# Kernel optimization log

Measured on AMD Instinct MI355X. Metric: run time of the kernel, lower is better.

Reference implementation:

```python
import jax, jax.numpy as jnp
import numpy as np
import math

B, L, D, H, FF = 4, 1024, 1024, 16, 4096
DH = D // H
EPS = 1e-12


def layer_norm(x, gamma, beta):
    mean = x.mean(-1, keepdims=True)
    var = ((x - mean) ** 2).mean(-1, keepdims=True)  # biased var, matches unbiased=False
    return gamma * (x - mean) / jnp.sqrt(var + EPS) + beta


def setup_inputs() -> dict:
    key = jax.random.key(0)
    ks = jax.random.split(key, 16)
    s = 0.02
    return {
        "x": jax.random.normal(ks[0], (B, L, D), jnp.float32),
        "attn_bias": jax.random.uniform(ks[1], (B, L, L), jnp.float32),
        "src_mask": jax.random.randint(ks[2], (B, L), 0, 2, jnp.int32),
        "wq": jax.random.normal(ks[3], (D, D), jnp.float32) * s,
        "bq": jnp.zeros((D,), jnp.float32),
        "wk": jax.random.normal(ks[4], (D, D), jnp.float32) * s,
        "bk": jnp.zeros((D,), jnp.float32),
        "wv": jax.random.normal(ks[5], (D, D), jnp.float32) * s,
        "bv": jnp.zeros((D,), jnp.float32),
        "wo": jax.random.normal(ks[6], (D, D), jnp.float32) * s,
        "bo": jnp.zeros((D,), jnp.float32),
        "gamma1": jnp.ones((D,), jnp.float32),
        "beta1": jnp.zeros((D,), jnp.float32),
        "w1": jax.random.normal(ks[7], (D, FF), jnp.float32) * s,
        "b1": jnp.zeros((FF,), jnp.float32),
        "w2": jax.random.normal(ks[8], (FF, D), jnp.float32) * s,
        "b2": jnp.zeros((D,), jnp.float32),
        "gamma2": jnp.ones((D,), jnp.float32),
        "beta2": jnp.zeros((D,), jnp.float32),
    }


def reference(x, attn_bias, src_mask, wq, bq, wk, bk, wv, bv, wo, bo,
              gamma1, beta1, w1, b1, w2, b2, gamma2, beta2):
    # ---- multi-head attention with multiplicative bias + additive mask ----
    def split_heads(t):  # [B,L,D] -> [B,H,L,DH]
        return t.reshape(B, L, H, DH).transpose(0, 2, 1, 3)

    q = split_heads(x @ wq + bq)
    k = split_heads(x @ wk + bk)
    v = split_heads(x @ wv + bv)

    score = jnp.einsum('bhqd,bhkd->bhqk', q, k) / math.sqrt(DH)
    score = score * attn_bias[:, None, :, :]               # multiplicative bias
    score = jnp.where(src_mask[:, None, None, :] == 0, -10000.0, score)
    p = jax.nn.softmax(score, axis=-1)
    ctx = jnp.einsum('bhqk,bhkd->bhqd', p, v)
    ctx = ctx.transpose(0, 2, 1, 3).reshape(B, L, D)
    attn_out = ctx @ wo + bo

    h = layer_norm(x + attn_out, gamma1, beta1)

    # ---- position-wise FFN ----
    ffn = jax.nn.relu(h @ w1 + b1) @ w2 + b2
    out = layer_norm(h + ffn, gamma2, beta2)
    return out
```

## Files before the change

kernel.cpp:

```cpp
#include <hip/hip_runtime.h>
#include <hip/hip_bf16.h>
#include <math.h>

#define BB 4
#define LL 1024
#define DD 1024
#define HH 16
#define DHH 64
#define FFF 4096
#define MM (BB*LL)
#define LDQ 3072

typedef __attribute__((ext_vector_type(8))) short short8;
typedef __attribute__((ext_vector_type(4))) float f32x4;

__device__ __forceinline__ ushort f2bf(float f) {
    __hip_bfloat16 h = __float2bfloat16(f);
    return *(ushort*)&h;
}
__device__ __forceinline__ float bf2f(ushort u) {
    __hip_bfloat16 h = *(__hip_bfloat16*)&u;
    return __bfloat162float(h);
}

__device__ __forceinline__ float block_reduce_sum(float v, float* red, int tid) {
    red[tid] = v;
    __syncthreads();
    for (int off = 128; off > 0; off >>= 1) {
        if (tid < off) red[tid] += red[tid + off];
        __syncthreads();
    }
    float r = red[0];
    __syncthreads();
    return r;
}

__global__ __launch_bounds__(256)
void cast_bf16(const float* __restrict__ in, ushort* __restrict__ out) {
    const int i = blockIdx.x * 256 + threadIdx.x;
    float4 v = ((const float4*)in)[i];
    ushort4 o;
    o.x = f2bf(v.x); o.y = f2bf(v.y); o.z = f2bf(v.z); o.w = f2bf(v.w);
    ((ushort4*)out)[i] = o;
}

__global__ __launch_bounds__(256)
void transpose_cast(const float* __restrict__ W, ushort* __restrict__ WT,
                    int K, int N) {
    __shared__ float tile[32][33];
    const int n0 = blockIdx.x * 32, k0 = blockIdx.y * 32;
    const int t = threadIdx.x;
    const int r = t >> 3, c4 = (t & 7) * 4;
    float4 v = *(const float4*)&W[(size_t)(k0 + r) * N + n0 + c4];
    tile[r][c4 + 0] = v.x; tile[r][c4 + 1] = v.y;
    tile[r][c4 + 2] = v.z; tile[r][c4 + 3] = v.w;
    __syncthreads();
    ushort4 o;
    o.x = f2bf(tile[c4 + 0][r]);
    o.y = f2bf(tile[c4 + 1][r]);
    o.z = f2bf(tile[c4 + 2][r]);
    o.w = f2bf(tile[c4 + 3][r]);
    *(ushort4*)&WT[(size_t)(n0 + r) * K + k0 + c4] = o;
}

__global__ __launch_bounds__(256)
void concat3(const float* __restrict__ a, const float* __restrict__ b,
             const float* __restrict__ c, float* __restrict__ o) {
    const int i = blockIdx.x * 256 + threadIdx.x;
    o[i] = (i < 1024) ? a[i] : ((i < 2048) ? b[i - 1024] : c[i - 2048]);
}

template<int BN>
__global__ __launch_bounds__(256)
void gemm_bf16(const ushort* __restrict__ A, const ushort* __restrict__ Bt,
               const float* __restrict__ bias, void* __restrict__ C,
               ushort* __restrict__ Vt, int vn0,
               int M, int N, int K, int relu, int obf16, int qlim) {
    constexpr int JF = BN / 32;
    __shared__ ushort Als0[128 * 32];
    __shared__ ushort Als1[128 * 32];
    __shared__ ushort Bls0[BN * 32];
    __shared__ ushort Bls1[BN * 32];

    const int L = blockIdx.x + gridDim.x * blockIdx.y;
    const int xcd = L & 7;
    const int idx = L >> 3;
    const int mpx = gridDim.y >> 3;
    const int bm = (xcd * mpx + (idx % mpx)) * 128;
    const int bn = (idx / mpx) * BN;

    const int t = threadIdx.x;
    const int lane = t & 63;
    const int w = t >> 6;
    const int wm = (w >> 1) * 64;
    const int wn = (w & 1) * (BN / 2);
    const int fm = lane & 15;
    const int kg = lane >> 4;

    f32x4 acc[4][JF] = {};

    for (int k0 = 0; k0 < K; k0 += 64) {
        #pragma unroll
        for (int j = 0; j < 2; ++j) {
            const int chunk = j * 256 + t;
            const int row = chunk >> 2, kc = chunk & 3;
            const ushort* ga0 = A + (size_t)(bm + row) * K + k0 + kc * 8;
            __builtin_amdgcn_global_load_lds(
                (const __attribute__((address_space(1))) void*)ga0,
                (__attribute__((address_space(3))) void*)(Als0 + chunk * 8), 16, 0, 0);
            const ushort* ga1 = ga0 + 32;
            __builtin_amdgcn_global_load_lds(
                (const __attribute__((address_space(1))) void*)ga1,
                (__attribute__((address_space(3))) void*)(Als1 + chunk * 8), 16, 0, 0);
        }
        #pragma unroll
        for (int j = 0; j < BN / 64; ++j) {
            const int chunk = j * 256 + t;
            const int row = chunk >> 2, kc = chunk & 3;
            const ushort* gb0 = Bt + (size_t)(bn + row) * K + k0 + kc * 8;
            __builtin_amdgcn_global_load_lds(
                (const __attribute__((address_space(1))) void*)gb0,
                (__attribute__((address_space(3))) void*)(Bls0 + chunk * 8), 16, 0, 0);
            const ushort* gb1 = gb0 + 32;
            __builtin_amdgcn_global_load_lds(
                (const __attribute__((address_space(1))) void*)gb1,
                (__attribute__((address_space(3))) void*)(Bls1 + chunk * 8), 16, 0, 0);
        }
        __syncthreads();

        short8 af[4][2], bfr[JF][2];
        #pragma unroll
        for (int i = 0; i < 4; ++i) {
            af[i][0] = *(const short8*)&Als0[(wm + i * 16 + fm) * 32 + kg * 8];
            af[i][1] = *(const short8*)&Als1[(wm + i * 16 + fm) * 32 + kg * 8];
        }
        #pragma unroll
        for (int j = 0; j < JF; ++j) {
            bfr[j][0] = *(const short8*)&Bls0[(wn + j * 16 + fm) * 32 + kg * 8];
            bfr[j][1] = *(const short8*)&Bls1[(wn + j * 16 + fm) * 32 + kg * 8];
        }
        #pragma unroll
        for (int i = 0; i < 4; ++i)
            #pragma unroll
            for (int j = 0; j < JF; ++j) {
                acc[i][j] = __builtin_amdgcn_mfma_f32_16x16x32_bf16(
                    af[i][0], bfr[j][0], acc[i][j], 0, 0, 0);
                acc[i][j] = __builtin_amdgcn_mfma_f32_16x16x32_bf16(
                    af[i][1], bfr[j][1], acc[i][j], 0, 0, 0);
            }
        __syncthreads();
    }

    const int orow0 = (lane >> 4) * 4;
    const int ocol = lane & 15;
    #pragma unroll
    for (int j = 0; j < JF; ++j) {
        const int n = bn + wn + j * 16 + ocol;
        const float bv = bias[n];
        const bool isV = (bn + wn + j * 16) >= vn0;
        #pragma unroll
        for (int i = 0; i < 4; ++i) {
            const int m0 = bm + wm + i * 16 + orow0;
            if (isV) {
                ushort4 o;
                float v0 = acc[i][j][0] + bv, v1 = acc[i][j][1] + bv;
                float v2 = acc[i][j][2] + bv, v3 = acc[i][j][3] + bv;
                o.x = f2bf(v0); o.y = f2bf(v1); o.z = f2bf(v2); o.w = f2bf(v3);
                *(ushort4*)&Vt[((size_t)((m0 >> 10) << 10) + (n - vn0)) * 1024 + (m0 & 1023)] = o;
            } else {
                #pragma unroll
                for (int r = 0; r < 4; ++r) {
                    const int m = m0 + r;
                    float v = acc[i][j][r] + bv;
                    if (relu) v = fmaxf(v, 0.0f);
                    if (n < qlim) v *= 0.125f;
                    if (obf16)
                        ((ushort*)C)[(size_t)m * N + n] = f2bf(v);
                    else
                        ((float*)C)[(size_t)m * N + n] = v;
                }
            }
        }
    }
}

__global__ __launch_bounds__(256, 2)
void attn_mfma(const ushort* __restrict__ QKVb, const ushort* __restrict__ Vt,
               const ushort* __restrict__ biasb, const int* __restrict__ mask,
               ushort* __restrict__ ctx) {
    const int q0 = blockIdx.x * 128;
    const int h = blockIdx.y;
    const int b = blockIdx.z;
    const int t = threadIdx.x;
    const int lane = t & 63;
    const int w = t >> 6;
    const int g = lane >> 4;
    const int c = lane & 15;

    __shared__ ushort Qs[128 * 72];
    __shared__ ushort Ks[64 * 72];
    __shared__ ushort Vs[64 * 72];
    __shared__ ushort Bs[128 * 72];
    __shared__ ushort Ps[4][32 * 72];
    __shared__ int maskS[LL];

    #pragma unroll
    for (int i = 0; i < 4; ++i) {
        const int chunk = i * 256 + t;
        const int row = chunk >> 3, c8 = (chunk & 7) * 8;
        *(short8*)&Qs[row * 72 + c8] =
            *(const short8*)(QKVb + ((size_t)(b * LL + q0 + row)) * LDQ + h * DHH + c8);
    }
    ((int4*)maskS)[t] = ((const int4*)(mask + b * LL))[t];

    short8 pk[2], pv[2], pb[4];
    #pragma unroll
    for (int i = 0; i < 2; ++i) {
        const int chunk = i * 256 + t;
        const int row = chunk >> 3, c8 = (chunk & 7) * 8;
        pk[i] = *(const short8*)(QKVb + ((size_t)(b * LL + row)) * LDQ + 1024 + h * DHH + c8);
        pv[i] = *(const short8*)(Vt + ((size_t)((b * HH + h) * DHH + row)) * LL + c8);
    }
    #pragma unroll
    for (int i = 0; i < 4; ++i) {
        const int chunk = i * 256 + t;
        const int row = chunk >> 3, c8 = (chunk & 7) * 8;
        pb[i] = *(const short8*)(biasb + ((size_t)(b * LL + q0 + row)) * LL + c8);
    }
    __syncthreads();

    short8 aq[2][2];
    #pragma unroll
    for (int p = 0; p < 2; ++p) {
        aq[p][0] = *(const short8*)&Qs[(w * 32 + p * 16 + c) * 72 + g * 8];
        aq[p][1] = *(const short8*)&Qs[(w * 32 + p * 16 + c) * 72 + g * 8 + 32];
    }

    float m_pr[2][4], l_run[2][4];
    f32x4 acc_o[2][4] = {};
    #pragma unroll
    for (int p = 0; p < 2; ++p)
        #pragma unroll
        for (int r = 0; r < 4; ++r) { m_pr[p][r] = -3.4e38f; l_run[p][r] = 0.0f; }

    for (int kt = 0; kt < 16; ++kt) {
        #pragma unroll
        for (int i = 0; i < 2; ++i) {
            const int chunk = i * 256 + t;
            const int row = chunk >> 3, c8 = (chunk & 7) * 8;
            *(short8*)&Ks[row * 72 + c8] = pk[i];
            *(short8*)&Vs[row * 72 + c8] = pv[i];
        }
        #pragma unroll
        for (int i = 0; i < 4; ++i) {
            const int chunk = i * 256 + t;
            const int row = chunk >> 3, c8 = (chunk & 7) * 8;
            *(short8*)&Bs[row * 72 + c8] = pb[i];
        }
        __syncthreads();

        if (kt < 15) {
            const int k0n = (kt + 1) * 64;
            #pragma unroll
            for (int i = 0; i < 2; ++i) {
                const int chunk = i * 256 + t;
                const int row = chunk >> 3, c8 = (chunk & 7) * 8;
                pk[i] = *(const short8*)(QKVb + ((size_t)(b * LL + k0n + row)) * LDQ + 1024 + h * DHH + c8);
                pv[i] = *(const short8*)(Vt + ((size_t)((b * HH + h) * DHH + row)) * LL + k0n + c8);
            }
            #pragma unroll
            for (int i = 0; i < 4; ++i) {
                const int chunk = i * 256 + t;
                const int row = chunk >> 3, c8 = (chunk & 7) * 8;
                pb[i] = *(const short8*)(biasb + ((size_t)(b * LL + q0 + row)) * LL + k0n + c8);
            }
        }
        const int k0 = kt * 64;

        f32x4 accs[2][4] = {};
        #pragma unroll
        for (int j = 0; j < 4; ++j) {
            short8 bk0 = *(const short8*)&Ks[(j * 16 + c) * 72 + g * 8];
            short8 bk1 = *(const short8*)&Ks[(j * 16 + c) * 72 + g * 8 + 32];
            #pragma unroll
            for (int p = 0; p < 2; ++p) {
                accs[p][j] = __builtin_amdgcn_mfma_f32_16x16x32_bf16(aq[p][0], bk0, accs[p][j], 0, 0, 0);
                accs[p][j] = __builtin_amdgcn_mfma_f32_16x16x32_bf16(aq[p][1], bk1, accs[p][j], 0, 0, 0);
            }
        }

        int mk[4];
        #pragma unroll
        for (int j = 0; j < 4; ++j) mk[j] = maskS[k0 + j * 16 + c];

        #pragma unroll
        for (int p = 0; p < 2; ++p) {
            float sc[4][4];
            #pragma unroll
            for (int j = 0; j < 4; ++j)
                #pragma unroll
                for (int r = 0; r < 4; ++r) {
                    const float bw = bf2f(Bs[(w * 32 + p * 16 + 4 * g + r) * 72 + j * 16 + c]);
                    float v = accs[p][j][r] * bw;
                    sc[j][r] = (mk[j] == 0) ? -10000.0f : v;
                }

            float mt[4];
            #pragma unroll
            for (int r = 0; r < 4; ++r)
                mt[r] = fmaxf(fmaxf(sc[0][r], sc[1][r]), fmaxf(sc[2][r], sc[3][r]));
            #pragma unroll
            for (int d = 1; d < 16; d <<= 1)
                #pragma unroll
                for (int r = 0; r < 4; ++r)
                    mt[r] = fmaxf(mt[r], __shfl_xor(mt[r], d));

            float al[4], lt[4];
            #pragma unroll
            for (int r = 0; r < 4; ++r) {
                float mn = fmaxf(m_pr[p][r], mt[r]);
                al[r] = __expf(m_pr[p][r] - mn);
                m_pr[p][r] = mn;
                lt[r] = 0.0f;
            }

            #pragma unroll
            for (int j = 0; j < 4; ++j)
                #pragma unroll
                for (int r = 0; r < 4; ++r) {
                    float pe = __expf(sc[j][r] - m_pr[p][r]);
                    lt[r] += pe;
                    Ps[w][(p * 16 + 4 * g + r) * 72 + j * 16 + c] = f2bf(pe);
                }
            #pragma unroll
            for (int d = 1; d < 16; d <<= 1)
                #pragma unroll
                for (int r = 0; r < 4; ++r)
                    lt[r] += __shfl_xor(lt[r], d);
            #pragma unroll
            for (int r = 0; r < 4; ++r)
                l_run[p][r] = l_run[p][r] * al[r] + lt[r];

            #pragma unroll
            for (int j = 0; j < 4; ++j)
                #pragma unroll
                for (int r = 0; r < 4; ++r)
                    acc_o[p][j][r] *= al[r];
        }

        #pragma unroll
        for (int ks = 0; ks < 2; ++ks) {
            short8 ap[2];
            #pragma unroll
            for (int p = 0; p < 2; ++p)
                ap[p] = *(const short8*)&Ps[w][(p * 16 + c) * 72 + ks * 32 + g * 8];
            #pragma unroll
            for (int j = 0; j < 4; ++j) {
                short8 bv8 = *(const short8*)&Vs[(j * 16 + c) * 72 + ks * 32 + g * 8];
                #pragma unroll
                for (int p = 0; p < 2; ++p)
                    acc_o[p][j] = __builtin_amdgcn_mfma_f32_16x16x32_bf16(ap[p], bv8, acc_o[p][j], 0, 0, 0);
            }
        }
        __syncthreads();
    }

    #pragma unroll
    for (int p = 0; p < 2; ++p)
        #pragma unroll
        for (int r = 0; r < 4; ++r) {
            const float inv = 1.0f / l_run[p][r];
            #pragma unroll
            for (int j = 0; j < 4; ++j)
                ctx[((size_t)(b * LL + q0 + w * 32 + p * 16 + 4 * g + r)) * DD + h * DHH + j * 16 + c] =
                    f2bf(acc_o[p][j][r] * inv);
        }
}

__global__ __launch_bounds__(256)
void add_ln_kernel(const float* __restrict__ a, const float* __restrict__ bres,
                   const float* __restrict__ gamma, const float* __restrict__ beta,
                   float* __restrict__ out, ushort* __restrict__ outb) {
    const int row = blockIdx.x;
    const int tid = threadIdx.x;
    __shared__ float red[256];

    const size_t base = (size_t)row * DD;
    float v[4];
    float sum = 0.0f;
    #pragma unroll
    for (int i = 0; i < 4; ++i) {
        const int col = tid + i * 256;
        v[i] = a[base + col] + bres[base + col];
        sum += v[i];
    }
    const float mean = block_reduce_sum(sum, red, tid) * (1.0f / 1024.0f);
    float vs = 0.0f;
    #pragma unroll
    for (int i = 0; i < 4; ++i) {
        const float dlt = v[i] - mean;
        vs += dlt * dlt;
    }
    const float var = block_reduce_sum(vs, red, tid) * (1.0f / 1024.0f);
    const float rstd = rsqrtf(var + 1e-12f);
    #pragma unroll
    for (int i = 0; i < 4; ++i) {
        const int col = tid + i * 256;
        const float o = gamma[col] * (v[i] - mean) * rstd + beta[col];
        out[base + col] = o;
        if (outb) outb[base + col] = f2bf(o);
    }
}

extern "C" void kernel_launch(void* const* d_in, const int* in_sizes, int n_in,
                              void* d_out, int out_size, void* d_ws, size_t ws_size,
                              hipStream_t stream) {
    const float* x         = (const float*)d_in[0];
    const float* attn_bias = (const float*)d_in[1];
    const int*   src_mask  = (const int*)  d_in[2];
    const float* wq = (const float*)d_in[3];
    const float* bq = (const float*)d_in[4];
    const float* wk = (const float*)d_in[5];
    const float* bk = (const float*)d_in[6];
    const float* wv = (const float*)d_in[7];
    const float* bv = (const float*)d_in[8];
    const float* wo = (const float*)d_in[9];
    const float* bo = (const float*)d_in[10];
    const float* gamma1 = (const float*)d_in[11];
    const float* beta1  = (const float*)d_in[12];
    const float* w1 = (const float*)d_in[13];
    const float* b1 = (const float*)d_in[14];
    const float* w2 = (const float*)d_in[15];
    const float* b2 = (const float*)d_in[16];
    const float* gamma2 = (const float*)d_in[17];
    const float* beta2  = (const float*)d_in[18];
    float* out = (float*)d_out;

    const size_t MB = 1024 * 1024;
    char* W = (char*)d_ws;
    ushort* xb    = (ushort*)(W + 0);
    ushort* ctxb  = (ushort*)(W + 0);
    ushort* QKVb  = (ushort*)(W + 8 * MB);
    ushort* F1b   = (ushort*)(W + 8 * MB);
    ushort* Vt    = (ushort*)(W + 40 * MB);
    ushort* W1T   = (ushort*)(W + 40 * MB);
    ushort* WQKVT = (ushort*)(W + 48 * MB);
    ushort* WOT   = (ushort*)(W + 48 * MB);
    ushort* Hbb   = (ushort*)(W + 54 * MB);
    ushort* W2T   = (ushort*)(W + 54 * MB);
    float*  bqkv  = (float*) (W + 62 * MB);
    ushort* biasb = (ushort*)(W + 64 * MB);
    float*  Ao    = (float*) (W + 64 * MB);
    float*  F2    = (float*) (W + 64 * MB);
    float*  Hb    = (float*) (W + 80 * MB);

    dim3 blk(256);

    cast_bf16<<<dim3(4096), blk, 0, stream>>>(x, xb);
    cast_bf16<<<dim3(4096), blk, 0, stream>>>(attn_bias, biasb);
    transpose_cast<<<dim3(32, 32), blk, 0, stream>>>(wq, WQKVT, DD, DD);
    transpose_cast<<<dim3(32, 32), blk, 0, stream>>>(wk, WQKVT + 1024 * 1024, DD, DD);
    transpose_cast<<<dim3(32, 32), blk, 0, stream>>>(wv, WQKVT + 2048 * 1024, DD, DD);
    concat3<<<dim3(12), blk, 0, stream>>>(bq, bk, bv, bqkv);
    gemm_bf16<128><<<dim3(24, 32), blk, 0, stream>>>(xb, WQKVT, bqkv, QKVb,
                                                     Vt, 2048, MM, LDQ, DD, 0, 1, 1024);
    attn_mfma<<<dim3(8, HH, BB), blk, 0, stream>>>(QKVb, Vt, biasb, src_mask, ctxb);
    transpose_cast<<<dim3(32, 32), blk, 0, stream>>>(wo, WOT, DD, DD);
    gemm_bf16<64><<<dim3(16, 32), blk, 0, stream>>>(ctxb, WOT, bo, Ao,
                                                    Vt, 1 << 30, MM, DD, DD, 0, 0, 0);
    add_ln_kernel<<<dim3(MM), blk, 0, stream>>>(Ao, x, gamma1, beta1, Hb, Hbb);
    transpose_cast<<<dim3(128, 32), blk, 0, stream>>>(w1, W1T, DD, FFF);
    gemm_bf16<128><<<dim3(32, 32), blk, 0, stream>>>(Hbb, W1T, b1, F1b,
                                                     Vt, 1 << 30, MM, FFF, DD, 1, 1, 0);
    transpose_cast<<<dim3(32, 128), blk, 0, stream>>>(w2, W2T, FFF, DD);
    gemm_bf16<64><<<dim3(16, 32), blk, 0, stream>>>(F1b, W2T, b2, F2,
                                                    Vt, 1 << 30, MM, DD, FFF, 0, 0, 0);
    add_ln_kernel<<<dim3(MM), blk, 0, stream>>>(F2, Hb, gamma2, beta2, out, nullptr);
}
```

Measured before the change: 419.8 us.

## Swizzle attention bias to fragment order and halve attention query tile

```diff
diff --git a/kernel.cpp b/kernel.cpp
--- a/kernel.cpp
+++ b/kernel.cpp
@@ -22,6 +22,13 @@
     __hip_bfloat16 h = *(__hip_bfloat16*)&u;
     return __bfloat162float(h);
 }
+__device__ __forceinline__ float fexp2(float x) {
+#if __has_builtin(__builtin_amdgcn_exp2f)
+    return __builtin_amdgcn_exp2f(x);
+#else
+    return exp2f(x);
+#endif
+}
 
 __device__ __forceinline__ float block_reduce_sum(float v, float* red, int tid) {
     red[tid] = v;
@@ -42,6 +49,23 @@
     ushort4 o;
     o.x = f2bf(v.x); o.y = f2bf(v.y); o.z = f2bf(v.z); o.w = f2bf(v.w);
     ((ushort4*)out)[i] = o;
+}
+
+__global__ __launch_bounds__(256)
+void swizzle_bias(const float* __restrict__ bias, ushort* __restrict__ B) {
+    __shared__ float rowbuf[1024];
+    const int row = blockIdx.x;
+    const int t = threadIdx.x;
+    *(float4*)&rowbuf[t * 4] = *(const float4*)&bias[(size_t)row * 1024 + t * 4];
+    __syncthreads();
+    const int kt = t >> 4, c = t & 15;
+    const float s = 1.4426950408889634f;
+    ushort4 o;
+    o.x = f2bf(rowbuf[kt * 64 + 0 * 16 + c] * s);
+    o.y = f2bf(rowbuf[kt * 64 + 1 * 16 + c] * s);
+    o.z = f2bf(rowbuf[kt * 64 + 2 * 16 + c] * s);
+    o.w = f2bf(rowbuf[kt * 64 + 3 * 16 + c] * s);
+    *(ushort4*)&B[(size_t)row * 1024 + t * 4] = o;
 }
 
 __global__ __launch_bounds__(256)
@@ -184,11 +208,11 @@
     }
 }
 
-__global__ __launch_bounds__(256, 2)
+__global__ __launch_bounds__(256, 3)
 void attn_mfma(const ushort* __restrict__ QKVb, const ushort* __restrict__ Vt,
-               const ushort* __restrict__ biasb, const int* __restrict__ mask,
+               const ushort* __restrict__ biasw, const int* __restrict__ mask,
                ushort* __restrict__ ctx) {
-    const int q0 = blockIdx.x * 128;
+    const int q0 = blockIdx.x * 64;
     const int h = blockIdx.y;
     const int b = blockIdx.z;
     const int t = threadIdx.x;
@@ -197,23 +221,21 @@
     const int g = lane >> 4;
     const int c = lane & 15;
 
-    __shared__ ushort Qs[128 * 72];
+    __shared__ ushort QP[64 * 72];
     __shared__ ushort Ks[64 * 72];
     __shared__ ushort Vs[64 * 72];
-    __shared__ ushort Bs[128 * 72];
-    __shared__ ushort Ps[4][32 * 72];
     __shared__ int maskS[LL];
 
     #pragma unroll
-    for (int i = 0; i < 4; ++i) {
+    for (int i = 0; i < 2; ++i) {
         const int chunk = i * 256 + t;
         const int row = chunk >> 3, c8 = (chunk & 7) * 8;
-        *(short8*)&Qs[row * 72 + c8] =
+        *(short8*)&QP[row * 72 + c8] =
             *(const short8*)(QKVb + ((size_t)(b * LL + q0 + row)) * LDQ + h * DHH + c8);
     }
     ((int4*)maskS)[t] = ((const int4*)(mask + b * LL))[t];
 
-    short8 pk[2], pv[2], pb[4];
+    short8 pk[2], pv[2];
     #pragma unroll
     for (int i = 0; i < 2; ++i) {
         const int chunk = i * 256 + t;
@@ -221,27 +243,15 @@
         pk[i] = *(const short8*)(QKVb + ((size_t)(b * LL + row)) * LDQ + 1024 + h * DHH + c8);
         pv[i] = *(const short8*)(Vt + ((size_t)((b * HH + h) * DHH + row)) * LL + c8);
     }
-    #pragma unroll
-    for (int i = 0; i < 4; ++i) {
-        const int chunk = i * 256 + t;
-        const int row = chunk >> 3, c8 = (chunk & 7) * 8;
-        pb[i] = *(const short8*)(biasb + ((size_t)(b * LL + q0 + row)) * LL + c8);
-    }
     __syncthreads();
 
-    short8 aq[2][2];
-    #pragma unroll
-    for (int p = 0; p < 2; ++p) {
-        aq[p][0] = *(const short8*)&Qs[(w * 32 + p * 16 + c) * 72 + g * 8];
-        aq[p][1] = *(const short8*)&Qs[(w * 32 + p * 16 + c) * 72 + g * 8 + 32];
-    }
-
-    float m_pr[2][4], l_run[2][4];
-    f32x4 acc_o[2][4] = {};
-    #pragma unroll
-    for (int p = 0; p < 2; ++p)
-        #pragma unroll
-        for (int r = 0; r < 4; ++r) { m_pr[p][r] = -3.4e38f; l_run[p][r] = 0.0f; }
+    short8 aq0 = *(const short8*)&QP[(w * 16 + c) * 72 + g * 8];
+    short8 aq1 = *(const short8*)&QP[(w * 16 + c) * 72 + g * 8 + 32];
+    ushort* Pw = QP + w * (16 * 72);
+
+    float m_pr[4] = {-3.4e38f, -3.4e38f, -3.4e38f, -3.4e38f};
+    float l_run[4] = {0.f, 0.f, 0.f, 0.f};
+    f32x4 acc_o[4] = {};
 
     for (int kt = 0; kt < 16; ++kt) {
         #pragma unroll
@@ -251,12 +261,6 @@
             *(short8*)&Ks[row * 72 + c8] = pk[i];
             *(short8*)&Vs[row * 72 + c8] = pv[i];
         }
-        #pragma unroll
-        for (int i = 0; i < 4; ++i) {
-            const int chunk = i * 256 + t;
-            const int row = chunk >> 3, c8 = (chunk & 7) * 8;
-            *(short8*)&Bs[row * 72 + c8] = pb[i];
-        }
         __syncthreads();
 
         if (kt < 15) {
@@ -268,113 +272,102 @@
                 pk[i] = *(const short8*)(QKVb + ((size_t)(b * LL + k0n + row)) * LDQ + 1024 + h * DHH + c8);
                 pv[i] = *(const short8*)(Vt + ((size_t)((b * HH + h) * DHH + row)) * LL + k0n + c8);
             }
-            #pragma unroll
-            for (int i = 0; i < 4; ++i) {
-                const int chunk = i * 256 + t;
-                const int row = chunk >> 3, c8 = (chunk & 7) * 8;
-                pb[i] = *(const short8*)(biasb + ((size_t)(b * LL + q0 + row)) * LL + k0n + c8);
-            }
-        }
-        const int k0 = kt * 64;
-
-        f32x4 accs[2][4] = {};
+        }
+
+        ushort4 pb[4];
+        #pragma unroll
+        for (int r = 0; r < 4; ++r) {
+            const int q = q0 + w * 16 + 4 * g + r;
+            pb[r] = *(const ushort4*)&biasw[((size_t)(b * LL + q) * 16 + kt) * 64 + c * 4];
+        }
+        int mk[4];
+        #pragma unroll
+        for (int j = 0; j < 4; ++j) mk[j] = maskS[kt * 64 + j * 16 + c];
+
+        f32x4 accs[4] = {};
         #pragma unroll
         for (int j = 0; j < 4; ++j) {
             short8 bk0 = *(const short8*)&Ks[(j * 16 + c) * 72 + g * 8];
             short8 bk1 = *(const short8*)&Ks[(j * 16 + c) * 72 + g * 8 + 32];
-            #pragma unroll
-            for (int p = 0; p < 2; ++p) {
-                accs[p][j] = __builtin_amdgcn_mfma_f32_16x16x32_bf16(aq[p][0], bk0, accs[p][j], 0, 0, 0);
-                accs[p][j] = __builtin_amdgcn_mfma_f32_16x16x32_bf16(aq[p][1], bk1, accs[p][j], 0, 0, 0);
-            }
-        }
-
-        int mk[4];
-        #pragma unroll
-        for (int j = 0; j < 4; ++j) mk[j] = maskS[k0 + j * 16 + c];
-
-        #pragma unroll
-        for (int p = 0; p < 2; ++p) {
-            float sc[4][4];
-            #pragma unroll
-            for (int j = 0; j < 4; ++j)
-                #pragma unroll
-                for (int r = 0; r < 4; ++r) {
-                    const float bw = bf2f(Bs[(w * 32 + p * 16 + 4 * g + r) * 72 + j * 16 + c]);
-                    float v = accs[p][j][r] * bw;
-                    sc[j][r] = (mk[j] == 0) ? -10000.0f : v;
-                }
-
-            float mt[4];
+            accs[j] = __builtin_amdgcn_mfma_f32_16x16x32_bf16(aq0, bk0, accs[j], 0, 0, 0);
+            accs[j] = __builtin_amdgcn_mfma_f32_16x16x32_bf16(aq1, bk1, accs[j], 0, 0, 0);
+        }
+
+        float sc[4][4];
+        #pragma unroll
+        for (int j = 0; j < 4; ++j)
+            #pragma unroll
+            for (int r = 0; r < 4; ++r) {
+                const float bw = bf2f(((const ushort*)&pb[r])[j]);
+                const float v = accs[j][r] * bw;
+                sc[j][r] = (mk[j] == 0) ? -14427.0f : v;
+            }
+
+        float mt[4];
+        #pragma unroll
+        for (int r = 0; r < 4; ++r)
+            mt[r] = fmaxf(fmaxf(sc[0][r], sc[1][r]), fmaxf(sc[2][r], sc[3][r]));
+        #pragma unroll
+        for (int d = 1; d < 16; d <<= 1)
             #pragma unroll
             for (int r = 0; r < 4; ++r)
-                mt[r] = fmaxf(fmaxf(sc[0][r], sc[1][r]), fmaxf(sc[2][r], sc[3][r]));
-            #pragma unroll
-            for (int d = 1; d < 16; d <<= 1)
-                #pragma unroll
-                for (int r = 0; r < 4; ++r)
-                    mt[r] = fmaxf(mt[r], __shfl_xor(mt[r], d));
-
-            float al[4], lt[4];
+                mt[r] = fmaxf(mt[r], __shfl_xor(mt[r], d));
+
+        float al[4], lt[4];
+        #pragma unroll
+        for (int r = 0; r < 4; ++r) {
+            const float mn = fmaxf(m_pr[r], mt[r]);
+            al[r] = fexp2(m_pr[r] - mn);
+            m_pr[r] = mn;
+            lt[r] = 0.0f;
+        }
+
+        #pragma unroll
+        for (int j = 0; j < 4; ++j)
             #pragma unroll
             for (int r = 0; r < 4; ++r) {
-                float mn = fmaxf(m_pr[p][r], mt[r]);
-                al[r] = __expf(m_pr[p][r] - mn);
-                m_pr[p][r] = mn;
-                lt[r] = 0.0f;
-            }
-
-            #pragma unroll
-            for (int j = 0; j < 4; ++j)
-                #pragma unroll
-                for (int r = 0; r < 4; ++r) {
-                    float pe = __expf(sc[j][r] - m_pr[p][r]);
-                    lt[r] += pe;
-                    Ps[w][(p * 16 + 4 * g + r) * 72 + j * 16 + c] = f2bf(pe);
-                }
-            #pragma unroll
-            for (int d = 1; d < 16; d <<= 1)
-                #pragma unroll
-                for (int r = 0; r < 4; ++r)
-                    lt[r] += __shfl_xor(lt[r], d);
-            #pragma unroll
-            for (int r = 0; r < 4; ++r)
-                l_run[p][r] = l_run[p][r] * al[r] + lt[r];
-
+                const float pe = fexp2(sc[j][r] - m_pr[r]);
+                lt[r] += pe;
+                Pw[(4 * g + r) * 72 + j * 16 + c] = f2bf(pe);
+            }
+
+        const bool ones = (al[0] == 1.0f) & (al[1] == 1.0f) &
+                          (al[2] == 1.0f) & (al[3] == 1.0f);
+        if (!__all(ones)) {
+            #pragma unroll
+            for (int r = 0; r < 4; ++r) l_run[r] *= al[r];
             #pragma unroll
             for (int j = 0; j < 4; ++j)
                 #pragma unroll
                 for (int r = 0; r < 4; ++r)
-                    acc_o[p][j][r] *= al[r];
-        }
+                    acc_o[j][r] *= al[r];
+        }
+        #pragma unroll
+        for (int r = 0; r < 4; ++r) l_run[r] += lt[r];
 
         #pragma unroll
         for (int ks = 0; ks < 2; ++ks) {
-            short8 ap[2];
-            #pragma unroll
-            for (int p = 0; p < 2; ++p)
-                ap[p] = *(const short8*)&Ps[w][(p * 16 + c) * 72 + ks * 32 + g * 8];
+            short8 ap = *(const short8*)&Pw[c * 72 + ks * 32 + g * 8];
             #pragma unroll
             for (int j = 0; j < 4; ++j) {
                 short8 bv8 = *(const short8*)&Vs[(j * 16 + c) * 72 + ks * 32 + g * 8];
-                #pragma unroll
-                for (int p = 0; p < 2; ++p)
-                    acc_o[p][j] = __builtin_amdgcn_mfma_f32_16x16x32_bf16(ap[p], bv8, acc_o[p][j], 0, 0, 0);
+                acc_o[j] = __builtin_amdgcn_mfma_f32_16x16x32_bf16(ap, bv8, acc_o[j], 0, 0, 0);
             }
         }
         __syncthreads();
     }
 
     #pragma unroll
-    for (int p = 0; p < 2; ++p)
-        #pragma unroll
-        for (int r = 0; r < 4; ++r) {
-            const float inv = 1.0f / l_run[p][r];
-            #pragma unroll
-            for (int j = 0; j < 4; ++j)
-                ctx[((size_t)(b * LL + q0 + w * 32 + p * 16 + 4 * g + r)) * DD + h * DHH + j * 16 + c] =
-                    f2bf(acc_o[p][j][r] * inv);
-        }
+    for (int r = 0; r < 4; ++r) {
+        float l = l_run[r];
+        #pragma unroll
+        for (int d = 1; d < 16; d <<= 1) l += __shfl_xor(l, d);
+        const float inv = 1.0f / l;
+        #pragma unroll
+        for (int j = 0; j < 4; ++j)
+            ctx[((size_t)(b * LL + q0 + w * 16 + 4 * g + r)) * DD + h * DHH + j * 16 + c] =
+                f2bf(acc_o[j][r] * inv);
+    }
 }
 
 __global__ __launch_bounds__(256)
@@ -449,7 +442,7 @@
     ushort* Hbb   = (ushort*)(W + 54 * MB);
     ushort* W2T   = (ushort*)(W + 54 * MB);
     float*  bqkv  = (float*) (W + 62 * MB);
-    ushort* biasb = (ushort*)(W + 64 * MB);
+    ushort* biasw = (ushort*)(W + 64 * MB);
     float*  Ao    = (float*) (W + 64 * MB);
     float*  F2    = (float*) (W + 64 * MB);
     float*  Hb    = (float*) (W + 80 * MB);
@@ -457,14 +450,14 @@
     dim3 blk(256);
 
     cast_bf16<<<dim3(4096), blk, 0, stream>>>(x, xb);
-    cast_bf16<<<dim3(4096), blk, 0, stream>>>(attn_bias, biasb);
+    swizzle_bias<<<dim3(4096), blk, 0, stream>>>(attn_bias, biasw);
     transpose_cast<<<dim3(32, 32), blk, 0, stream>>>(wq, WQKVT, DD, DD);
     transpose_cast<<<dim3(32, 32), blk, 0, stream>>>(wk, WQKVT + 1024 * 1024, DD, DD);
     transpose_cast<<<dim3(32, 32), blk, 0, stream>>>(wv, WQKVT + 2048 * 1024, DD, DD);
     concat3<<<dim3(12), blk, 0, stream>>>(bq, bk, bv, bqkv);
     gemm_bf16<128><<<dim3(24, 32), blk, 0, stream>>>(xb, WQKVT, bqkv, QKVb,
                                                      Vt, 2048, MM, LDQ, DD, 0, 1, 1024);
-    attn_mfma<<<dim3(8, HH, BB), blk, 0, stream>>>(QKVb, Vt, biasb, src_mask, ctxb);
+    attn_mfma<<<dim3(16, HH, BB), blk, 0, stream>>>(QKVb, Vt, biasw, src_mask, ctxb);
     transpose_cast<<<dim3(32, 32), blk, 0, stream>>>(wo, WOT, DD, DD);
     gemm_bf16<64><<<dim3(16, 32), blk, 0, stream>>>(ctxb, WOT, bo, Ao,
                                                     Vt, 1 << 30, MM, DD, DD, 0, 0, 0);
```

Measured after the change: 400.6 us. -4.6%, faster.
